# Performance work log

Hardware: AMD Instinct MI355X
Metric: run time of the kernel (lower is better)

## Reference

```python
import jax, jax.numpy as jnp
import numpy as np

HEADS = 2
OUT_CH = 128
NEG_SLOPE_ATT = 0.2   # GATv2Conv attention LeakyReLU
NEG_SLOPE_ACT = 0.01  # nn.LeakyReLU default
BN_EPS = 1e-5


def setup_inputs() -> dict:
    key = jax.random.key(0)
    ks = jax.random.split(key, 8)
    B, C, D, H, W = 2, 128, 8, 32, 32
    N = B * D * H * W            # 16384 graph nodes
    E = 196608                   # avg degree 12
    x = jax.random.normal(ks[0], (B, C, D, H, W), dtype=jnp.float32)
    edge_index = jax.random.randint(ks[1], (2, E), 0, N, dtype=jnp.int64)
    lin_w = jax.random.normal(ks[2], (C, HEADS * OUT_CH), dtype=jnp.float32) * (1.0 / np.sqrt(C))
    lin_b = jax.random.normal(ks[3], (HEADS * OUT_CH,), dtype=jnp.float32) * 0.02
    att = jax.random.normal(ks[4], (HEADS, OUT_CH), dtype=jnp.float32) * (1.0 / np.sqrt(OUT_CH))
    gat_bias = jax.random.normal(ks[5], (OUT_CH,), dtype=jnp.float32) * 0.02
    bn_gamma = jnp.ones((OUT_CH,), dtype=jnp.float32)
    bn_beta = jnp.zeros((OUT_CH,), dtype=jnp.float32)
    return {"x": x, "edge_index": edge_index, "lin_w": lin_w, "lin_b": lin_b,
            "att": att, "gat_bias": gat_bias, "bn_gamma": bn_gamma, "bn_beta": bn_beta}


def _gatv2(xf, src, dst, lin_w, lin_b, att, gat_bias, n_nodes):
    # shared-weights GATv2: x' = x W + b, per edge e=(j->i): score = a . lrelu(x'_i + x'_j)
    h = (xf @ lin_w + lin_b).reshape(n_nodes, HEADS, OUT_CH)  # [N, H, C]
    x_src = h[src]                                            # [E, H, C] messages
    logits = jnp.einsum('ehc,hc->eh', jax.nn.leaky_relu(x_src + h[dst], NEG_SLOPE_ATT), att)
    # segment softmax over edges sharing the same target node
    m = jax.ops.segment_max(logits, dst, num_segments=n_nodes)      # [N, H]
    ex = jnp.exp(logits - m[dst])
    denom = jax.ops.segment_sum(ex, dst, num_segments=n_nodes)      # [N, H]
    alpha = ex / denom[dst]
    out = jax.ops.segment_sum(x_src * alpha[..., None], dst, num_segments=n_nodes)  # [N, H, C]
    return out.mean(axis=1) + gat_bias  # concat=False -> head mean


def reference(x, edge_index, lin_w, lin_b, att, gat_bias, bn_gamma, bn_beta):
    B, C, D, H, W = x.shape
    N = B * D * H * W
    xf = x.reshape(B, C, -1).transpose(0, 2, 1).reshape(N, C)
    # add_self_loops=True (PyG default)
    loop = jnp.arange(N, dtype=edge_index.dtype)
    src = jnp.concatenate([edge_index[0], loop])
    dst = jnp.concatenate([edge_index[1], loop])
    out = _gatv2(xf, src, dst, lin_w, lin_b, att, gat_bias, N)      # [N, OUT_CH]
    out = out.reshape(B, D * H * W, OUT_CH).transpose(0, 2, 1).reshape(B, OUT_CH, D, H, W)
    # BatchNorm3d (training-mode batch stats, biased variance)
    mean = out.mean(axis=(0, 2, 3, 4), keepdims=True)
    var = out.var(axis=(0, 2, 3, 4), keepdims=True)
    out = (out - mean) / jnp.sqrt(var + BN_EPS)
    out = out * bn_gamma.reshape(1, -1, 1, 1, 1) + bn_beta.reshape(1, -1, 1, 1, 1)
    return jax.nn.leaky_relu(out, NEG_SLOPE_ACT)
```

## Files before the change

### kernel.cpp

```cpp
#include <hip/hip_runtime.h>
#include <math.h>

#define N_NODES 16384
#define CIN 128
#define HOUT 256
#define OUTC 128
#define NEG_ATT 0.2f
#define NEG_ACT 0.01f
#define BN_EPS 1e-5f

typedef short short8 __attribute__((ext_vector_type(8)));
typedef float f32x4 __attribute__((ext_vector_type(4)));

static __device__ __forceinline__ unsigned short f2bf(float f) {
    unsigned int u = __float_as_uint(f);
    unsigned int r = (u + 0x7FFFu + ((u >> 16) & 1u)) >> 16;
    return (unsigned short)r;
}
static __device__ __forceinline__ float bf2f(unsigned short s) {
    return __uint_as_float(((unsigned int)s) << 16);
}

#define LDP 136
__global__ __launch_bounds__(256) void gemm_kernel(const float* __restrict__ x,
                                                   const float* __restrict__ lin_w,
                                                   const float* __restrict__ lin_b,
                                                   unsigned short* __restrict__ h,
                                                   int* __restrict__ deg,
                                                   float* __restrict__ gz) {
    __shared__ __align__(16) unsigned short A_s[64 * LDP];
    __shared__ __align__(16) unsigned short Bt_s[64 * LDP];
    const int t = threadIdx.x;
    const int bid = blockIdx.x;

    if (t < 16) deg[bid * 16 + t] = 0;
    if (bid == 0) gz[t] = 0.f;

    const int node0 = (bid >> 2) * 64;
    const int o0 = (bid & 3) * 64;
    const int b = node0 >> 13;
    const int s0 = node0 & 8191;

    const int nt = t & 15;
    const int kt = t >> 4;
#pragma unroll
    for (int p = 0; p < 2; p++) {
        const int kb = p * 64 + kt * 4;
        float4 ar[4], br[4];
#pragma unroll
        for (int r = 0; r < 4; r++) {
            ar[r] = *(const float4*)&x[((b * CIN + kb + r) << 13) + s0 + nt * 4];
            br[r] = *(const float4*)&lin_w[(kb + r) * HOUT + o0 + nt * 4];
        }
#pragma unroll
        for (int j = 0; j < 4; j++) {
            ushort4 va, vb;
            va.x = f2bf(((const float*)&ar[0])[j]);
            va.y = f2bf(((const float*)&ar[1])[j]);
            va.z = f2bf(((const float*)&ar[2])[j]);
            va.w = f2bf(((const float*)&ar[3])[j]);
            vb.x = f2bf(((const float*)&br[0])[j]);
            vb.y = f2bf(((const float*)&br[1])[j]);
            vb.z = f2bf(((const float*)&br[2])[j]);
            vb.w = f2bf(((const float*)&br[3])[j]);
            *(ushort4*)&A_s[(nt * 4 + j) * LDP + kb] = va;
            *(ushort4*)&Bt_s[(nt * 4 + j) * LDP + kb] = vb;
        }
    }
    __syncthreads();

    const int w = t >> 6;
    const int lane = t & 63;
    const int lrow = lane & 15;
    const int lquad = lane >> 4;
    const int m0 = w * 16;

    short8 afr[4];
#pragma unroll
    for (int ks = 0; ks < 4; ks++)
        afr[ks] = *(const short8*)&A_s[(m0 + lrow) * LDP + ks * 32 + lquad * 8];

    f32x4 acc[4];
#pragma unroll
    for (int c = 0; c < 4; c++) { acc[c][0] = 0.f; acc[c][1] = 0.f; acc[c][2] = 0.f; acc[c][3] = 0.f; }

#pragma unroll
    for (int c = 0; c < 4; c++) {
#pragma unroll
        for (int ks = 0; ks < 4; ks++) {
            short8 bfr = *(const short8*)&Bt_s[(c * 16 + lrow) * LDP + ks * 32 + lquad * 8];
            acc[c] = __builtin_amdgcn_mfma_f32_16x16x32_bf16(afr[ks], bfr, acc[c], 0, 0, 0);
        }
    }

#pragma unroll
    for (int c = 0; c < 4; c++) {
        const int col = o0 + c * 16 + lrow;
        const float lb = lin_b[col];
#pragma unroll
        for (int r = 0; r < 4; r++) {
            const int n = node0 + m0 + lquad * 4 + r;
            h[n * HOUT + col] = f2bf(acc[c][r] + lb);
        }
    }
}

__global__ void count_kernel(const int* __restrict__ dst, int* __restrict__ deg, int E) {
    int e = blockIdx.x * 256 + threadIdx.x;
    if (e < E) atomicAdd(&deg[dst[e]], 1);
}

__global__ __launch_bounds__(1024) void scan_kernel(const int* __restrict__ deg,
                                                    int* __restrict__ row_ptr,
                                                    int* __restrict__ cursor) {
    __shared__ int sums[1024];
    const int t = threadIdx.x;
    int local[16];
    int s = 0;
#pragma unroll
    for (int k = 0; k < 16; k++) {
        local[k] = deg[t * 16 + k];
        s += local[k];
    }
    sums[t] = s;
    __syncthreads();
    for (int off = 1; off < 1024; off <<= 1) {
        int v = (t >= off) ? sums[t - off] : 0;
        __syncthreads();
        sums[t] += v;
        __syncthreads();
    }
    int run = sums[t] - s;
#pragma unroll
    for (int k = 0; k < 16; k++) {
        row_ptr[t * 16 + k] = run;
        cursor[t * 16 + k] = run;
        run += local[k];
    }
    if (t == 1023) row_ptr[N_NODES] = run;
}

__global__ void scatter_kernel(const int* __restrict__ edges, int* __restrict__ cursor,
                               int* __restrict__ csr, int E) {
    int e = blockIdx.x * 256 + threadIdx.x;
    if (e < E) {
        int s = edges[e];
        int d = edges[E + e];
        int p = atomicAdd(&cursor[d], 1);
        csr[p] = s;
    }
}

__global__ __launch_bounds__(256) void gat_kernel(const unsigned short* __restrict__ h,
                                                  const int* __restrict__ row_ptr,
                                                  const int* __restrict__ csr,
                                                  const float* __restrict__ att,
                                                  const float* __restrict__ gat_bias,
                                                  float* __restrict__ gat,
                                                  float* __restrict__ gsum,
                                                  float* __restrict__ gsumsq) {
    const int t = threadIdx.x;
    const int lane = t & 63;
    const int w = t >> 6;
    __shared__ float ssum[128], ssq[128];
    if (t < 128) { ssum[t] = 0.f; ssq[t] = 0.f; }
    __syncthreads();

    const ushort4* __restrict__ h4 = (const ushort4*)h;
    float4 a4 = ((const float4*)att)[lane];
    float4 gb = ((const float4*)gat_bias)[lane & 31];
    float st[4] = {0.f, 0.f, 0.f, 0.f}, sq[4] = {0.f, 0.f, 0.f, 0.f};

    for (int i = 0; i < 4; i++) {
        const int node = (blockIdx.x << 4) + (w << 2) + i;
        ushort4 hd4 = h4[(node << 6) + lane];
        float hdx = bf2f(hd4.x), hdy = bf2f(hd4.y), hdz = bf2f(hd4.z), hdw = bf2f(hd4.w);
        const int beg = row_ptr[node];
        const int cnt = row_ptr[node + 1] - beg + 1;
        float m = -INFINITY, denom = 0.f;
        float4 acc = make_float4(0.f, 0.f, 0.f, 0.f);

        for (int base = 0; base < cnt; base += 8) {
            int j[8];
#pragma unroll
            for (int u = 0; u < 8; u++) {
                int e = base + u;
                j[u] = (e == 0 || e >= cnt) ? node : csr[beg + e - 1];
            }
            float4 hj[8];
            float p[8];
#pragma unroll
            for (int u = 0; u < 8; u++) {
                ushort4 hv = h4[(j[u] << 6) + lane];
                hj[u].x = bf2f(hv.x); hj[u].y = bf2f(hv.y);
                hj[u].z = bf2f(hv.z); hj[u].w = bf2f(hv.w);
                float vx = hj[u].x + hdx; vx = vx > 0.f ? vx : NEG_ATT * vx;
                float vy = hj[u].y + hdy; vy = vy > 0.f ? vy : NEG_ATT * vy;
                float vz = hj[u].z + hdz; vz = vz > 0.f ? vz : NEG_ATT * vz;
                float vw = hj[u].w + hdw; vw = vw > 0.f ? vw : NEG_ATT * vw;
                p[u] = vx * a4.x + vy * a4.y + vz * a4.z + vw * a4.w;
            }
#pragma unroll
            for (int s = 1; s <= 16; s <<= 1) {
#pragma unroll
                for (int u = 0; u < 8; u++) p[u] += __shfl_xor(p[u], s);
            }
#pragma unroll
            for (int u = 0; u < 8; u++)
                if (base + u >= cnt) p[u] = -INFINITY;
            float nm = m;
#pragma unroll
            for (int u = 0; u < 8; u++) nm = fmaxf(nm, p[u]);
            float scale = __expf(m - nm);
            float wt[8];
#pragma unroll
            for (int u = 0; u < 8; u++) wt[u] = __expf(p[u] - nm);
            float wsum = 0.f;
#pragma unroll
            for (int u = 0; u < 8; u++) wsum += wt[u];
            denom = denom * scale + wsum;
            float ax = acc.x * scale, ay = acc.y * scale, az = acc.z * scale, aw = acc.w * scale;
#pragma unroll
            for (int u = 0; u < 8; u++) {
                ax = fmaf(wt[u], hj[u].x, ax);
                ay = fmaf(wt[u], hj[u].y, ay);
                az = fmaf(wt[u], hj[u].z, az);
                aw = fmaf(wt[u], hj[u].w, aw);
            }
            acc.x = ax; acc.y = ay; acc.z = az; acc.w = aw;
            m = nm;
        }
        float inv = 1.0f / denom;
        float rx = acc.x * inv, ry = acc.y * inv, rz = acc.z * inv, rw = acc.w * inv;
        rx += __shfl_xor(rx, 32);
        ry += __shfl_xor(ry, 32);
        rz += __shfl_xor(rz, 32);
        rw += __shfl_xor(rw, 32);
        if (lane < 32) {
            float4 o;
            o.x = 0.5f * rx + gb.x;
            o.y = 0.5f * ry + gb.y;
            o.z = 0.5f * rz + gb.z;
            o.w = 0.5f * rw + gb.w;
            ((float4*)gat)[(node << 5) + lane] = o;
            st[0] += o.x; sq[0] += o.x * o.x;
            st[1] += o.y; sq[1] += o.y * o.y;
            st[2] += o.z; sq[2] += o.z * o.z;
            st[3] += o.w; sq[3] += o.w * o.w;
        }
    }
    if (lane < 32) {
#pragma unroll
        for (int c = 0; c < 4; c++) {
            atomicAdd(&ssum[(lane << 2) + c], st[c]);
            atomicAdd(&ssq[(lane << 2) + c], sq[c]);
        }
    }
    __syncthreads();
    if (t < 128) {
        atomicAdd(&gsum[t], ssum[t]);
        atomicAdd(&gsumsq[t], ssq[t]);
    }
}

__global__ __launch_bounds__(256) void epilogue_kernel(const float* __restrict__ gat,
                                                       const float* __restrict__ gsum,
                                                       const float* __restrict__ gsumsq,
                                                       const float* __restrict__ gamma,
                                                       const float* __restrict__ beta,
                                                       float* __restrict__ out) {
    __shared__ float tile[64 * 129];
    __shared__ float sc[128], sh[128];
    const int t = threadIdx.x;
    if (t < 128) {
        const float invN = 1.0f / (float)N_NODES;
        float mean = gsum[t] * invN;
        float var = gsumsq[t] * invN - mean * mean;
        float rstd = rsqrtf(var + BN_EPS);
        float s = gamma[t] * rstd;
        sc[t] = s;
        sh[t] = beta[t] - mean * s;
    }
    __syncthreads();
    const int n0 = blockIdx.x * 64;
    const int b = n0 >> 13;
    const int s0 = n0 & 8191;
#pragma unroll
    for (int k = 0; k < 32; k++) {
        int f = t + k * 256;
        int nl = f >> 7;
        int c = f & 127;
        float v = gat[(n0 << 7) + f];
        v = v * sc[c] + sh[c];
        v = v > 0.f ? v : NEG_ACT * v;
        tile[nl * 129 + c] = v;
    }
    __syncthreads();
    const int sl = t & 63;
    const int c0 = t >> 6;
#pragma unroll
    for (int k = 0; k < 32; k++) {
        int c = c0 + (k << 2);
        out[((b * OUTC + c) << 13) + s0 + sl] = tile[sl * 129 + c];
    }
}

extern "C" void kernel_launch(void* const* d_in, const int* in_sizes, int n_in,
                              void* d_out, int out_size, void* d_ws, size_t ws_size,
                              hipStream_t stream) {
    const float* x        = (const float*)d_in[0];
    const int*   edges    = (const int*)d_in[1];
    const float* lin_w    = (const float*)d_in[2];
    const float* lin_b    = (const float*)d_in[3];
    const float* att      = (const float*)d_in[4];
    const float* gat_bias = (const float*)d_in[5];
    const float* bn_gamma = (const float*)d_in[6];
    const float* bn_beta  = (const float*)d_in[7];
    float* out = (float*)d_out;
    int E = in_sizes[1] / 2;

    char* ws = (char*)d_ws;
    unsigned short* h = (unsigned short*)(ws);
    float* gat     = (float*)(ws + 8388608);
    int*   deg     = (int*)(ws + 16777216);
    int*   row_ptr = (int*)(ws + 16842752);
    int*   cursor  = (int*)(ws + 16908544);
    int*   csr     = (int*)(ws + 16974080);
    float* gsum    = (float*)(ws + 17825792);
    float* gsumsq  = gsum + 128;

    gemm_kernel<<<1024, 256, 0, stream>>>(x, lin_w, lin_b, h, deg, gsum);
    count_kernel<<<(E + 255) / 256, 256, 0, stream>>>(edges + E, deg, E);
    scan_kernel<<<1, 1024, 0, stream>>>(deg, row_ptr, cursor);
    scatter_kernel<<<(E + 255) / 256, 256, 0, stream>>>(edges, cursor, csr, E);
    gat_kernel<<<N_NODES / 16, 256, 0, stream>>>(h, row_ptr, csr, att, gat_bias, gat, gsum, gsumsq);
    epilogue_kernel<<<N_NODES / 64, 256, 0, stream>>>(gat, gsum, gsumsq, bn_gamma, bn_beta, out);
}
```

Measured before the change: 164.3 us.

## Split GAT wave into half-waves over edges with 16-byte loads, drop running max

```diff
diff --git a/kernel.cpp b/kernel.cpp
--- a/kernel.cpp
+++ b/kernel.cpp
@@ -19,6 +19,17 @@
 }
 static __device__ __forceinline__ float bf2f(unsigned short s) {
     return __uint_as_float(((unsigned int)s) << 16);
+}
+static __device__ __forceinline__ void loadbf8(const unsigned short* p, float* f) {
+    uint4 u = *(const uint4*)p;
+    f[0] = __uint_as_float(u.x << 16);
+    f[1] = __uint_as_float(u.x & 0xffff0000u);
+    f[2] = __uint_as_float(u.y << 16);
+    f[3] = __uint_as_float(u.y & 0xffff0000u);
+    f[4] = __uint_as_float(u.z << 16);
+    f[5] = __uint_as_float(u.z & 0xffff0000u);
+    f[6] = __uint_as_float(u.w << 16);
+    f[7] = __uint_as_float(u.w & 0xffff0000u);
 }
 
 #define LDP 136
@@ -162,98 +173,93 @@
     const int t = threadIdx.x;
     const int lane = t & 63;
     const int w = t >> 6;
+    const int half = lane >> 5;
+    const int sub = lane & 31;
+    const int c0 = sub * 8;
+
     __shared__ float ssum[128], ssq[128];
     if (t < 128) { ssum[t] = 0.f; ssq[t] = 0.f; }
     __syncthreads();
 
-    const ushort4* __restrict__ h4 = (const ushort4*)h;
-    float4 a4 = ((const float4*)att)[lane];
-    float4 gb = ((const float4*)gat_bias)[lane & 31];
-    float st[4] = {0.f, 0.f, 0.f, 0.f}, sq[4] = {0.f, 0.f, 0.f, 0.f};
+    float av[8];
+    *(float4*)&av[0] = *(const float4*)&att[c0];
+    *(float4*)&av[4] = *(const float4*)&att[c0 + 4];
+    float gb[8];
+    *(float4*)&gb[0] = *(const float4*)&gat_bias[c0 & 127];
+    *(float4*)&gb[4] = *(const float4*)&gat_bias[(c0 & 127) + 4];
+
+    float st[8] = {}, sq[8] = {};
 
     for (int i = 0; i < 4; i++) {
         const int node = (blockIdx.x << 4) + (w << 2) + i;
-        ushort4 hd4 = h4[(node << 6) + lane];
-        float hdx = bf2f(hd4.x), hdy = bf2f(hd4.y), hdz = bf2f(hd4.z), hdw = bf2f(hd4.w);
+        float hd[8];
+        loadbf8(&h[node * HOUT + c0], hd);
         const int beg = row_ptr[node];
-        const int cnt = row_ptr[node + 1] - beg + 1;
-        float m = -INFINITY, denom = 0.f;
-        float4 acc = make_float4(0.f, 0.f, 0.f, 0.f);
-
-        for (int base = 0; base < cnt; base += 8) {
-            int j[8];
-#pragma unroll
-            for (int u = 0; u < 8; u++) {
-                int e = base + u;
-                j[u] = (e == 0 || e >= cnt) ? node : csr[beg + e - 1];
-            }
-            float4 hj[8];
-            float p[8];
-#pragma unroll
-            for (int u = 0; u < 8; u++) {
-                ushort4 hv = h4[(j[u] << 6) + lane];
-                hj[u].x = bf2f(hv.x); hj[u].y = bf2f(hv.y);
-                hj[u].z = bf2f(hv.z); hj[u].w = bf2f(hv.w);
-                float vx = hj[u].x + hdx; vx = vx > 0.f ? vx : NEG_ATT * vx;
-                float vy = hj[u].y + hdy; vy = vy > 0.f ? vy : NEG_ATT * vy;
-                float vz = hj[u].z + hdz; vz = vz > 0.f ? vz : NEG_ATT * vz;
-                float vw = hj[u].w + hdw; vw = vw > 0.f ? vw : NEG_ATT * vw;
-                p[u] = vx * a4.x + vy * a4.y + vz * a4.z + vw * a4.w;
-            }
-#pragma unroll
-            for (int s = 1; s <= 16; s <<= 1) {
-#pragma unroll
-                for (int u = 0; u < 8; u++) p[u] += __shfl_xor(p[u], s);
-            }
-#pragma unroll
-            for (int u = 0; u < 8; u++)
-                if (base + u >= cnt) p[u] = -INFINITY;
-            float nm = m;
-#pragma unroll
-            for (int u = 0; u < 8; u++) nm = fmaxf(nm, p[u]);
-            float scale = __expf(m - nm);
-            float wt[8];
-#pragma unroll
-            for (int u = 0; u < 8; u++) wt[u] = __expf(p[u] - nm);
-            float wsum = 0.f;
-#pragma unroll
-            for (int u = 0; u < 8; u++) wsum += wt[u];
-            denom = denom * scale + wsum;
-            float ax = acc.x * scale, ay = acc.y * scale, az = acc.z * scale, aw = acc.w * scale;
-#pragma unroll
-            for (int u = 0; u < 8; u++) {
-                ax = fmaf(wt[u], hj[u].x, ax);
-                ay = fmaf(wt[u], hj[u].y, ay);
-                az = fmaf(wt[u], hj[u].z, az);
-                aw = fmaf(wt[u], hj[u].w, aw);
-            }
-            acc.x = ax; acc.y = ay; acc.z = az; acc.w = aw;
-            m = nm;
-        }
+        const int cntT = row_ptr[node + 1] - beg + 1;
+        float denom = 0.f;
+        float acc[8] = {};
+
+        for (int base = 0; base < cntT; base += 8) {
+            int ei[4];
+            int jj[4];
+#pragma unroll
+            for (int u = 0; u < 4; u++) {
+                ei[u] = base + 2 * u + half;
+                jj[u] = (ei[u] == 0) ? node : ((ei[u] < cntT) ? csr[beg + ei[u] - 1] : node);
+            }
+            float hj[4][8];
+            float p[4];
+#pragma unroll
+            for (int u = 0; u < 4; u++) {
+                loadbf8(&h[jj[u] * HOUT + c0], hj[u]);
+                float d = 0.f;
+#pragma unroll
+                for (int c = 0; c < 8; c++) {
+                    float v = hj[u][c] + hd[c];
+                    v = fmaxf(v, NEG_ATT * v);
+                    d = fmaf(v, av[c], d);
+                }
+                p[u] = d;
+            }
+#pragma unroll
+            for (int s = 1; s <= 8; s <<= 1) {
+#pragma unroll
+                for (int u = 0; u < 4; u++) p[u] += __shfl_xor(p[u], s);
+            }
+#pragma unroll
+            for (int u = 0; u < 4; u++) {
+                float wt = (ei[u] < cntT) ? __expf(p[u]) : 0.f;
+                denom += wt;
+#pragma unroll
+                for (int c = 0; c < 8; c++) acc[c] = fmaf(wt, hj[u][c], acc[c]);
+            }
+        }
+        denom += __shfl_xor(denom, 32);
+#pragma unroll
+        for (int c = 0; c < 8; c++) acc[c] += __shfl_xor(acc[c], 32);
         float inv = 1.0f / denom;
-        float rx = acc.x * inv, ry = acc.y * inv, rz = acc.z * inv, rw = acc.w * inv;
-        rx += __shfl_xor(rx, 32);
-        ry += __shfl_xor(ry, 32);
-        rz += __shfl_xor(rz, 32);
-        rw += __shfl_xor(rw, 32);
-        if (lane < 32) {
-            float4 o;
-            o.x = 0.5f * rx + gb.x;
-            o.y = 0.5f * ry + gb.y;
-            o.z = 0.5f * rz + gb.z;
-            o.w = 0.5f * rw + gb.w;
-            ((float4*)gat)[(node << 5) + lane] = o;
-            st[0] += o.x; sq[0] += o.x * o.x;
-            st[1] += o.y; sq[1] += o.y * o.y;
-            st[2] += o.z; sq[2] += o.z * o.z;
-            st[3] += o.w; sq[3] += o.w * o.w;
-        }
-    }
-    if (lane < 32) {
-#pragma unroll
-        for (int c = 0; c < 4; c++) {
-            atomicAdd(&ssum[(lane << 2) + c], st[c]);
-            atomicAdd(&ssq[(lane << 2) + c], sq[c]);
+        float r[8];
+#pragma unroll
+        for (int c = 0; c < 8; c++) r[c] = acc[c] * inv;
+#pragma unroll
+        for (int c = 0; c < 8; c++) r[c] += __shfl_xor(r[c], 16);
+        if (lane < 16) {
+            float o[8];
+#pragma unroll
+            for (int c = 0; c < 8; c++) {
+                o[c] = 0.5f * r[c] + gb[c];
+                st[c] += o[c];
+                sq[c] += o[c] * o[c];
+            }
+            *(float4*)&gat[node * OUTC + c0] = *(float4*)&o[0];
+            *(float4*)&gat[node * OUTC + c0 + 4] = *(float4*)&o[4];
+        }
+    }
+    if (lane < 16) {
+#pragma unroll
+        for (int c = 0; c < 8; c++) {
+            atomicAdd(&ssum[c0 + c], st[c]);
+            atomicAdd(&ssq[c0 + c], sq[c]);
         }
     }
     __syncthreads();
```

Measured after the change: 158.3 us. 1.04x faster.
